# Kernel tuning notes

Hardware: AMD Instinct MI355X
Metric: run time of the kernel (lower is better)

Reference implementation:

```python
import jax, jax.numpy as jnp
import numpy as np

B, L, D, H = 2, 2048, 2048, 16
HD = D // H          # head_dim = 128
LAT = HD // 4        # latent_dim = 32


def setup_inputs() -> dict:
    key = jax.random.key(0)
    ks = jax.random.split(key, 16)
    def w(k, shape, fan_in):
        return jax.random.normal(k, shape, jnp.float32) / np.float32(np.sqrt(fan_in))
    x = jax.random.normal(ks[0], (B, L, D), jnp.float32)
    # RoPE frequencies, stored as (cos, sin) pairs: [L, HD//2, 2]
    inv_freq = 1.0 / (10000.0 ** (np.arange(0, HD, 2, dtype=np.float32) / HD))
    ang = np.outer(np.arange(L, dtype=np.float32), inv_freq)
    freqs_cis = jnp.stack([jnp.asarray(np.cos(ang)), jnp.asarray(np.sin(ang))], axis=-1)
    return dict(
        x=x, freqs_cis=freqs_cis,
        Wq=w(ks[1], (D, D), D), bq=jnp.zeros((D,), jnp.float32),
        Wk=w(ks[2], (D, D), D), bk=jnp.zeros((D,), jnp.float32),
        Wv=w(ks[3], (D, D), D), bv=jnp.zeros((D,), jnp.float32),
        Wqc=w(ks[4], (LAT, HD), HD), bqc=jnp.zeros((LAT,), jnp.float32),
        Wkc=w(ks[5], (LAT, HD), HD), bkc=jnp.zeros((LAT,), jnp.float32),
        Wvc=w(ks[6], (LAT, HD), HD), bvc=jnp.zeros((LAT,), jnp.float32),
        Wd=w(ks[7], (HD, LAT), LAT), bd=jnp.zeros((HD,), jnp.float32),
        Wo=w(ks[8], (D, D), D), bo=jnp.zeros((D,), jnp.float32),
    )


def _rope(t, freqs_cis):
    # t: [B,H,L,HD]; freqs_cis: [L, HD//2, 2] (cos, sin)
    tp = t.reshape(t.shape[:-1] + (HD // 2, 2))
    a, b = tp[..., 0], tp[..., 1]
    cr = freqs_cis[:, :, 0]  # [L, HD//2]
    ci = freqs_cis[:, :, 1]
    ra = a * cr - b * ci
    rb = a * ci + b * cr
    return jnp.stack([ra, rb], axis=-1).reshape(t.shape)


def reference(x, freqs_cis, Wq, bq, Wk, bk, Wv, bv, Wqc, bqc, Wkc, bkc, Wvc, bvc, Wd, bd, Wo, bo):
    Bx, Lx, Dx = x.shape
    # QKV projections -> [B,H,L,HD]
    def proj(W, bias):
        return (x @ W.T + bias).reshape(Bx, Lx, H, HD).transpose(0, 2, 1, 3)
    q = proj(Wq, bq)
    k = proj(Wk, bk)
    v = proj(Wv, bv)
    q = _rope(q, freqs_cis)
    k = _rope(k, freqs_cis)
    # per-head compression to latent dim: [B,H,L,LAT]
    qc = q @ Wqc.T + bqc
    kc = k @ Wkc.T + bkc
    vc = v @ Wvc.T + bvc
    scores = jnp.einsum('bhie,bhje->bhij', qc, kc) / np.float32(np.sqrt(LAT))
    mask = jnp.triu(jnp.ones((Lx, Lx), bool), 1)  # future positions
    scores = jnp.where(mask, jnp.float32(-jnp.inf), scores)
    probs = jax.nn.softmax(scores, axis=-1)
    attn = jnp.einsum('bhij,bhje->bhie', probs, vc)  # [B,H,L,LAT]
    attn = attn @ Wd.T + bd                          # decompress -> [B,H,L,HD]
    attn = attn.transpose(0, 2, 1, 3).reshape(Bx, Lx, Dx)
    return attn @ Wo.T + bo
```

## Files before the change

### kernel.cpp

```cpp
#include <hip/hip_runtime.h>

typedef __attribute__((ext_vector_type(8))) __bf16 bf16x8;
typedef __attribute__((ext_vector_type(4))) __bf16 bf16x4;
typedef __attribute__((ext_vector_type(4))) float f32x4;
typedef __attribute__((ext_vector_type(16))) float f32x16;

#define LL 2048
#define DD 2048
#define HH 16
#define HDIM 128

__global__ __launch_bounds__(256)
void cvt_all(const float* __restrict__ x, const float* __restrict__ Wq,
             const float* __restrict__ Wk, const float* __restrict__ Wqc,
             const float* __restrict__ Wkc,
             __bf16* __restrict__ xb, __bf16* __restrict__ Wqb, __bf16* __restrict__ Wkb,
             __bf16* __restrict__ Wqcb, __bf16* __restrict__ Wkcb)
{
    size_t i = (size_t)blockIdx.x * 256 + threadIdx.x;
    const float* s; __bf16* d; size_t off;
    if (i < 2097152)      { s = x;   d = xb;   off = i; }
    else if (i < 3145728) { s = Wq;  d = Wqb;  off = i - 2097152; }
    else if (i < 4194304) { s = Wk;  d = Wkb;  off = i - 3145728; }
    else if (i < 4195328) { s = Wqc; d = Wqcb; off = i - 4194304; }
    else                  { s = Wkc; d = Wkcb; off = i - 4195328; }
    float4 v = *(const float4*)(s + off * 4);
    bf16x4 o = { (__bf16)v.x, (__bf16)v.y, (__bf16)v.z, (__bf16)v.w };
    *(bf16x4*)(d + off * 4) = o;
}

__global__ __launch_bounds__(256)
void build_wv_eff(const float* __restrict__ Wv, const float* __restrict__ Wvc,
                  const float* __restrict__ bv, const float* __restrict__ bvc,
                  __bf16* __restrict__ Wveff, float* __restrict__ bveff)
{
    __shared__ float WvcT[128][32];
    const int h = blockIdx.x, dc = blockIdx.y, tid = threadIdx.x;
    for (int i = tid; i < 4096; i += 256) WvcT[i & 127][i >> 7] = Wvc[i];
    __syncthreads();
    const int d  = dc * 64 + (tid & 63);
    const int o0 = (tid >> 6) * 8;
    float acc[8] = {};
    for (int j = 0; j < 128; ++j) {
        const float w = Wv[(size_t)(h * 128 + j) * 2048 + d];
        #pragma unroll
        for (int o = 0; o < 8; ++o) acc[o] += WvcT[j][o0 + o] * w;
    }
    #pragma unroll
    for (int o = 0; o < 8; ++o)
        Wveff[(size_t)(h * 32 + o0 + o) * 2048 + d] = (__bf16)acc[o];
    if (dc == 0 && tid < 32) {
        float s = bvc[tid];
        for (int j = 0; j < 128; ++j) s += WvcT[j][tid] * bv[h * 128 + j];
        bveff[h * 32 + tid] = s;
    }
}

__global__ __launch_bounds__(256)
void build_wo_eff(const float* __restrict__ Wo, const float* __restrict__ Wd,
                  __bf16* __restrict__ Woeff)
{
    __shared__ float WdL[128][32];
    const int dc = blockIdx.x, h = blockIdx.y, tid = threadIdx.x;
    for (int i = tid; i < 4096; i += 256) WdL[i >> 5][i & 31] = Wd[i];
    __syncthreads();
    const int dout = dc * 64 + (tid & 63);
    const int o0   = (tid >> 6) * 8;
    float acc[8] = {};
    const float* wrow = Wo + (size_t)dout * 2048 + h * 128;
    for (int u = 0; u < 128; ++u) {
        const float w = wrow[u];
        #pragma unroll
        for (int o = 0; o < 8; ++o) acc[o] += WdL[u][o0 + o] * w;
    }
    #pragma unroll
    for (int o = 0; o < 8; ++o)
        Woeff[(size_t)dout * 512 + h * 32 + o0 + o] = (__bf16)acc[o];
}

__global__ __launch_bounds__(256)
void build_bo_eff(const float* __restrict__ Wo, const float* __restrict__ bd,
                  const float* __restrict__ bo, float* __restrict__ boeff)
{
    __shared__ float bdL[128];
    const int tid = threadIdx.x;
    if (tid < 128) bdL[tid] = bd[tid];
    __syncthreads();
    const int d  = blockIdx.x * 32 + (tid >> 3);
    const int s0 = (tid & 7) * 64;
    float s = 0.f;
    const float* wrow = Wo + (size_t)d * 2048 + s0 * 4;
    for (int c4 = 0; c4 < 64; ++c4) {
        float4 wv = *(const float4*)(wrow + c4 * 4);
        const int cb = ((s0 + c4) * 4) & 127;
        s += wv.x * bdL[cb] + wv.y * bdL[cb + 1] + wv.z * bdL[cb + 2] + wv.w * bdL[cb + 3];
    }
    #pragma unroll
    for (int off = 4; off; off >>= 1) s += __shfl_down(s, off, 8);
    if ((tid & 7) == 0) boeff[d] = bo[d] + s;
}

typedef unsigned int u32;
typedef const __attribute__((address_space(1))) u32* gp_t;
typedef __attribute__((address_space(3))) u32* lp_t;
__device__ __forceinline__ void gload16(const __bf16* g, __bf16* l)
{
    __builtin_amdgcn_global_load_lds((gp_t)(const void*)g, (lp_t)(void*)l, 16, 0, 0);
}

#define MF16(a, b, c) __builtin_amdgcn_mfma_f32_16x16x32_bf16(a, b, c, 0, 0, 0)

__global__ __launch_bounds__(256, 3)
void gemm_qkv(const __bf16* __restrict__ A,
              const __bf16* __restrict__ Wq, const __bf16* __restrict__ Wk,
              const __bf16* __restrict__ Wveff,
              const float* __restrict__ bq, const float* __restrict__ bk,
              const float* __restrict__ bveff,
              __bf16* __restrict__ qb, __bf16* __restrict__ kb, __bf16* __restrict__ vt)
{
    __shared__ __bf16 lds[3][2][4096];

    const int bid = blockIdx.x;
    const int xcd = bid & 7;
    const int j   = bid >> 3;
    const int bx  = j >> 2;
    const int byl = j & 3;
    const int by  = xcd * 4 + byl;
    const int m0  = by * 128;
    const int which = (bx >= 32) ? 2 : (bx >> 4);
    const int n0  = (which == 2) ? (bx - 32) * 128 : (bx & 15) * 128;
    const __bf16* W = which == 0 ? Wq : which == 1 ? Wk : Wveff;

    const int tid  = threadIdx.x;
    const int wid  = tid >> 6;
    const int lane = tid & 63;
    const int wr   = wid >> 1;
    const int wc   = wid & 1;
    const int l15  = lane & 15;
    const int l4   = lane >> 4;
    const int swz  = (l4 ^ (l15 & 3)) * 8;

    const int srl  = lane >> 2;
    const int scol = ((lane & 3) ^ (srl & 3)) * 8;
    const __bf16* gA0 = A + (size_t)(m0 + wid * 32 + srl) * 2048 + scol;
    const __bf16* gB0 = W + (size_t)(n0 + wid * 32 + srl) * 2048 + scol;

    #define STAGE(bb, kk)                                                \
    {   __bf16* dA = &lds[bb][0][wid * 1024];                            \
        __bf16* dB = &lds[bb][1][wid * 1024];                            \
        gload16(gA0 + (kk), dA);                                         \
        gload16(gA0 + (size_t)16 * 2048 + (kk), dA + 512);               \
        gload16(gB0 + (kk), dB);                                         \
        gload16(gB0 + (size_t)16 * 2048 + (kk), dB + 512);               \
    }
    #define RD_A(bb, mf) (*(const bf16x8*)&lds[bb][0][(wr * 64 + (mf) * 16 + l15) * 32 + swz])
    #define RD_B(bb, nf) (*(const bf16x8*)&lds[bb][1][(wc * 64 + (nf) * 16 + l15) * 32 + swz])

    f32x4 acc[4][4] = {};

    STAGE(0, 0) STAGE(1, 32)
    asm volatile("s_waitcnt vmcnt(4)" ::: "memory");
    __builtin_amdgcn_s_barrier();

    #define TB(RB, SB, VM, DOST, kk)                                          \
    {                                                                         \
        bf16x8 fa[4], fb[4];                                                  \
        fa[0] = RD_A(RB, 0); fa[1] = RD_A(RB, 1);                             \
        fa[2] = RD_A(RB, 2); fa[3] = RD_A(RB, 3);                             \
        fb[0] = RD_B(RB, 0); fb[1] = RD_B(RB, 1);                             \
        fb[2] = RD_B(RB, 2); fb[3] = RD_B(RB, 3);                             \
        if (DOST) STAGE(SB, kk)                                               \
        asm volatile("s_waitcnt lgkmcnt(0)" ::: "memory");                    \
        __builtin_amdgcn_sched_barrier(0);                                    \
        __builtin_amdgcn_s_setprio(1);                                        \
        _Pragma("unroll")                                                     \
        for (int mf = 0; mf < 4; ++mf)                                        \
            _Pragma("unroll")                                                 \
            for (int nf = 0; nf < 4; ++nf)                                    \
                acc[mf][nf] = MF16(fa[mf], fb[nf], acc[mf][nf]);              \
        __builtin_amdgcn_s_setprio(0);                                        \
        asm volatile("s_waitcnt vmcnt(" VM ")" ::: "memory");                 \
        __builtin_amdgcn_s_barrier();                                         \
    }

    for (int tt = 0; tt < 60; tt += 3) {
        const int kk = (tt + 2) * 32;
        TB(0, 2, "4", true, kk)
        TB(1, 0, "4", true, kk + 32)
        TB(2, 1, "4", true, kk + 64)
    }
    TB(0, 2, "4", true, 62 * 32)
    TB(1, 0, "4", true, 63 * 32)
    TB(2, 0, "0", false, 0)
    TB(0, 0, "0", false, 0)
    #undef TB
    #undef STAGE
    #undef RD_A
    #undef RD_B

    if (which < 2) {
        __bf16* C = which ? kb : qb;
        const float* bb = which ? bk : bq;
        #pragma unroll
        for (int nf = 0; nf < 4; ++nf) {
            const int col = n0 + wc * 64 + nf * 16 + l15;
            const float bv = bb[col];
            #pragma unroll
            for (int mf = 0; mf < 4; ++mf) {
                const int row0 = m0 + wr * 64 + mf * 16 + l4 * 4;
                #pragma unroll
                for (int rr = 0; rr < 4; ++rr)
                    C[(size_t)(row0 + rr) * 2048 + col] = (__bf16)(acc[mf][nf][rr] + bv);
            }
        }
    } else {
        #pragma unroll
        for (int nf = 0; nf < 4; ++nf) {
            const int ncol = n0 + wc * 64 + nf * 16 + l15;
            const float bv = bveff[ncol];
            const int hh = ncol >> 5, oo = ncol & 31;
            #pragma unroll
            for (int mf = 0; mf < 4; ++mf) {
                const int row0 = m0 + wr * 64 + mf * 16 + l4 * 4;
                const int b = row0 >> 11, l0 = row0 & 2047;
                bf16x4 pk = { (__bf16)(acc[mf][nf][0] + bv), (__bf16)(acc[mf][nf][1] + bv),
                              (__bf16)(acc[mf][nf][2] + bv), (__bf16)(acc[mf][nf][3] + bv) };
                *(bf16x4*)(vt + ((size_t)((b * 16 + hh) * 32 + oo)) * 2048 + l0) = pk;
            }
        }
    }
}

__global__ __launch_bounds__(256)
void gemm_ao(const __bf16* __restrict__ ao, const __bf16* __restrict__ Woeff,
             const float* __restrict__ boeff, float* __restrict__ out)
{
    __shared__ __bf16 As[128][64];
    __shared__ __bf16 Bs[128][64];
    const int bid = blockIdx.x;
    const int x   = bid & 7;
    const int jj  = bid >> 3;
    const int bx  = x * 2 + (jj & 1);
    const int by  = jj >> 1;
    const int m0  = by * 128;
    const int n0  = bx * 128;

    const int tid  = threadIdx.x;
    const int wave = tid >> 6;
    const int lane = tid & 63;
    const int wr   = (wave >> 1) * 64;
    const int wc   = (wave & 1) * 64;
    const int lr   = lane & 15;
    const int lk   = (lane >> 4) * 8;
    const int srow = wave * 32 + (lane >> 3);
    const int scol = (lane & 7) * 8;

    f32x4 acc[4][4] = {};
    __bf16* lA = &As[wave * 32][0];
    __bf16* lB = &Bs[wave * 32][0];
    const __bf16* Ww = Woeff + (size_t)(n0 + srow) * 512 + scol;

    for (int k0 = 0; k0 < 512; k0 += 64) {
        const int kk = k0 + scol;
        const int hblk = kk >> 5, oo = kk & 31;
        #pragma unroll
        for (int j = 0; j < 4; ++j) {
            const int r = m0 + srow + j * 8;
            const int b = r >> 11, l = r & 2047;
            gload16(ao + ((size_t)((b << 4) + hblk) * 2048 + l) * 32 + oo, lA + j * 512);
            gload16(Ww + (size_t)(j * 8) * 512 + k0, lB + j * 512);
        }
        __syncthreads();
        #pragma unroll
        for (int ks = 0; ks < 2; ++ks) {
            bf16x8 af[4], bfr[4];
            #pragma unroll
            for (int m = 0; m < 4; ++m)
                af[m] = *(const bf16x8*)(&As[wr + m * 16 + lr][ks * 32 + lk]);
            #pragma unroll
            for (int n = 0; n < 4; ++n)
                bfr[n] = *(const bf16x8*)(&Bs[wc + n * 16 + lr][ks * 32 + lk]);
            #pragma unroll
            for (int m = 0; m < 4; ++m)
                #pragma unroll
                for (int n = 0; n < 4; ++n)
                    acc[m][n] = MF16(af[m], bfr[n], acc[m][n]);
        }
        __syncthreads();
    }

    const int orow = (lane >> 4) * 4;
    #pragma unroll
    for (int n = 0; n < 4; ++n) {
        const int col = n0 + wc + n * 16 + lr;
        const float bv = boeff[col];
        #pragma unroll
        for (int m = 0; m < 4; ++m) {
            #pragma unroll
            for (int r = 0; r < 4; ++r) {
                const int row = m0 + wr + m * 16 + orow + r;
                out[(size_t)row * 2048 + col] = acc[m][n][r] + bv;
            }
        }
    }
}

__global__ __launch_bounds__(256)
void latproj_mfma(const __bf16* __restrict__ qb, const __bf16* __restrict__ kb,
                  const __bf16* __restrict__ Wqcb, const __bf16* __restrict__ Wkcb,
                  const float* __restrict__ bq, const float* __restrict__ bk,
                  const float* __restrict__ fc,
                  __bf16* __restrict__ qc, __bf16* __restrict__ kc)
{
    const int which = blockIdx.y;
    const __bf16* in = which == 0 ? qb : kb;
    const __bf16* Wb = which == 0 ? Wqcb : Wkcb;
    const float*  bs = which == 0 ? bq : bk;

    const int wave = threadIdx.x >> 6;
    const int lane = threadIdx.x & 63;
    const int o    = lane & 31;
    const int hi   = lane >> 5;
    const int g0   = (blockIdx.x * 4 + wave) * 32;

    bf16x8 wf[8];
    #pragma unroll
    for (int ks = 0; ks < 8; ++ks)
        wf[ks] = *(const bf16x8*)(Wb + o * 128 + ks * 16 + hi * 8);

    const int g = g0 + o;
    const int b = g >> 15, h = (g >> 11) & 15, l = g & (LL - 1);
    const __bf16* arow = in + ((size_t)(b * LL + l)) * DD + h * HDIM;
    const float* fcr = fc + (size_t)l * 128;

    f32x16 C = {};
    #pragma unroll
    for (int ks = 0; ks < 8; ++ks) {
        bf16x8 af = *(const bf16x8*)(arow + ks * 16 + hi * 8);
        const float4 cA = *(const float4*)(fcr + (ks * 8 + hi * 4) * 2);
        const float4 cB = *(const float4*)(fcr + (ks * 8 + hi * 4) * 2 + 4);
        float a, bb_;
        a = (float)af[0]; bb_ = (float)af[1];
        af[0] = (__bf16)(a * cA.x - bb_ * cA.y); af[1] = (__bf16)(a * cA.y + bb_ * cA.x);
        a = (float)af[2]; bb_ = (float)af[3];
        af[2] = (__bf16)(a * cA.z - bb_ * cA.w); af[3] = (__bf16)(a * cA.w + bb_ * cA.z);
        a = (float)af[4]; bb_ = (float)af[5];
        af[4] = (__bf16)(a * cB.x - bb_ * cB.y); af[5] = (__bf16)(a * cB.y + bb_ * cB.x);
        a = (float)af[6]; bb_ = (float)af[7];
        af[6] = (__bf16)(a * cB.z - bb_ * cB.w); af[7] = (__bf16)(a * cB.w + bb_ * cB.z);
        C = __builtin_amdgcn_mfma_f32_32x32x16_bf16(af, wf[ks], C, 0, 0, 0);
    }

    const float bias = bs[o];
    const float QSCALE = 0.17677669529663689f * 1.44269504088896340f;
    __bf16* outp = (which == 0 ? qc : kc);
    #pragma unroll
    for (int r = 0; r < 16; ++r) {
        const int ro = (r & 3) + 8 * (r >> 2) + 4 * hi;
        float v = C[r] + bias;
        if (which == 0) v *= QSCALE;
        outp[(size_t)(g0 + ro) * 32 + o] = (__bf16)v;
    }
}

__device__ __forceinline__ unsigned pkbf2(float a, float b)
{
    union { __bf16 h[2]; unsigned u; } x;
    x.h[0] = (__bf16)a; x.h[1] = (__bf16)b;
    return x.u;
}

#if __has_builtin(__builtin_amdgcn_permlane32_swap)
typedef unsigned int uint2v __attribute__((ext_vector_type(2)));
__device__ __forceinline__ void plswap(unsigned a, unsigned b, unsigned& w_lo, unsigned& w_hi, int)
{
    uint2v r = __builtin_amdgcn_permlane32_swap(a, b, false, false);
    w_lo = r[0]; w_hi = r[1];
}
#else
__device__ __forceinline__ void plswap(unsigned a, unsigned b, unsigned& w_lo, unsigned& w_hi, int hi)
{
    unsigned ax = (unsigned)__shfl_xor((int)a, 32);
    unsigned bx = (unsigned)__shfl_xor((int)b, 32);
    w_lo = hi ? bx : a;
    w_hi = hi ? b  : ax;
}
#endif

__global__ __launch_bounds__(64)
void attn_part(const __bf16* __restrict__ qc, const __bf16* __restrict__ kc,
               const __bf16* __restrict__ vt,
               float* __restrict__ pm, float* __restrict__ pl, float* __restrict__ po)
{
    const int id  = blockIdx.x;
    const int bhl = id & 7;
    const int c   = id >> 3;
    const int bhh = c / 160;
    const int lin = c - bhh * 160;
    int s, ci;
    if (lin < 16)      { s = lin; ci = 0; }
    else if (lin < 48) { int q = lin - 16; s = 16 + (q >> 1); ci = q & 1; }
    else if (lin < 96) { int q = lin - 48; int d = q / 3; s = 32 + d; ci = q - d * 3; }
    else               { int q = lin - 96; s = 48 + (q >> 2); ci = q & 3; }
    const int bh = bhh * 8 + bhl;

    const int lane = threadIdx.x;
    const int qcol = lane & 31;
    const int hi   = lane >> 5;

    const __bf16* qbase = qc + ((size_t)bh * LL + (size_t)s * 32) * 32;
    const __bf16* kbase = kc + (size_t)bh * LL * 32;
    const __bf16* vbase = vt + (size_t)bh * 32 * LL;

    const bf16x8 qf0 = *(const bf16x8*)(qbase + qcol * 32 + hi * 8);
    const bf16x8 qf1 = *(const bf16x8*)(qbase + qcol * 32 + 16 + hi * 8);

    float m = -1e30f, lsum = 0.f;
    f32x16 O = {};

    const int t0 = ci * 16;
    const int t1 = min(s, t0 + 15);

    const __bf16* krow = kbase + (size_t)(t0 * 32 + qcol) * 32 + hi * 8;
    const __bf16* vrow = vbase + (size_t)qcol * LL + t0 * 32 + hi * 8;
    bf16x8 kc0 = *(const bf16x8*)(krow);
    bf16x8 kc1 = *(const bf16x8*)(krow + 16);
    bf16x8 vc0 = *(const bf16x8*)(vrow);
    bf16x8 vc1 = *(const bf16x8*)(vrow + 16);

    for (int t = t0; t <= t1; ++t) {
        const int tn = (t < t1) ? t + 1 : t;
        const __bf16* krn = kbase + (size_t)(tn * 32 + qcol) * 32 + hi * 8;
        const __bf16* vrn = vbase + (size_t)qcol * LL + tn * 32 + hi * 8;
        bf16x8 kn0 = *(const bf16x8*)(krn);
        bf16x8 kn1 = *(const bf16x8*)(krn + 16);
        bf16x8 vn0 = *(const bf16x8*)(vrn);
        bf16x8 vn1 = *(const bf16x8*)(vrn + 16);

        f32x16 S = {};
        S = __builtin_amdgcn_mfma_f32_32x32x16_bf16(kc0, qf0, S, 0, 0, 0);
        S = __builtin_amdgcn_mfma_f32_32x32x16_bf16(kc1, qf1, S, 0, 0, 0);

        if (t == s) {
            #pragma unroll
            for (int r = 0; r < 16; ++r) {
                const int kl = (r & 3) + 8 * (r >> 2) + 4 * hi;
                if (kl > qcol) S[r] = -1e30f;
            }
        }
        float tm = S[0];
        #pragma unroll
        for (int r = 1; r < 16; ++r) tm = fmaxf(tm, S[r]);
        tm = fmaxf(tm, __shfl_xor(tm, 32));
        const float mn = fmaxf(m, tm);
        const float fr = exp2f(m - mn);
        m = mn;
        float p[16]; float ls = 0.f;
        #pragma unroll
        for (int r = 0; r < 16; ++r) { p[r] = exp2f(S[r] - m); ls += p[r]; }
        lsum = lsum * fr + ls;
        #pragma unroll
        for (int r = 0; r < 16; ++r) O[r] *= fr;

        unsigned w[8];
        #pragma unroll
        for (int i = 0; i < 8; ++i) w[i] = pkbf2(p[2 * i], p[2 * i + 1]);
        union PF { unsigned u[4]; bf16x8 v; } pf1, pf2;
        plswap(w[0], w[2], pf1.u[0], pf1.u[2], hi);
        plswap(w[1], w[3], pf1.u[1], pf1.u[3], hi);
        plswap(w[4], w[6], pf2.u[0], pf2.u[2], hi);
        plswap(w[5], w[7], pf2.u[1], pf2.u[3], hi);

        O = __builtin_amdgcn_mfma_f32_32x32x16_bf16(vc0, pf1.v, O, 0, 0, 0);
        O = __builtin_amdgcn_mfma_f32_32x32x16_bf16(vc1, pf2.v, O, 0, 0, 0);

        kc0 = kn0; kc1 = kn1; vc0 = vn0; vc1 = vn1;
    }

    const float L = lsum + __shfl_xor(lsum, 32);
    const size_t g = (size_t)bh * LL + (size_t)s * 32 + qcol;
    const size_t slot = g * 4 + ci;
    if (hi == 0) { pm[slot] = m; pl[slot] = L; }
    float* pp = po + slot * 32;
    #pragma unroll
    for (int g4 = 0; g4 < 4; ++g4) {
        float4 v = { O[g4 * 4 + 0], O[g4 * 4 + 1], O[g4 * 4 + 2], O[g4 * 4 + 3] };
        *(float4*)(pp + g4 * 8 + 4 * hi) = v;
    }
}

__global__ __launch_bounds__(256)
void attn_comb(const float* __restrict__ pm, const float* __restrict__ pl,
               const float* __restrict__ po, __bf16* __restrict__ ao)
{
    const int g = blockIdx.x * 256 + threadIdx.x;
    const int i = g & (LL - 1);
    const int nch = (i >> 9) + 1;
    float m = -1e30f;
    for (int c = 0; c < nch; ++c) m = fmaxf(m, pm[(size_t)g * 4 + c]);
    float L = 0.f;
    float o[32] = {};
    for (int c = 0; c < nch; ++c) {
        const float w = exp2f(pm[(size_t)g * 4 + c] - m);
        L += w * pl[(size_t)g * 4 + c];
        const float* pp = po + ((size_t)g * 4 + c) * 32;
        #pragma unroll
        for (int d4 = 0; d4 < 8; ++d4) {
            float4 v = *(const float4*)(pp + d4 * 4);
            o[d4*4+0] += w * v.x; o[d4*4+1] += w * v.y;
            o[d4*4+2] += w * v.z; o[d4*4+3] += w * v.w;
        }
    }
    const float inv = 1.f / L;
    #pragma unroll
    for (int d8 = 0; d8 < 4; ++d8) {
        bf16x8 v;
        #pragma unroll
        for (int j = 0; j < 8; ++j) v[j] = (__bf16)(o[d8 * 8 + j] * inv);
        *(bf16x8*)(ao + (size_t)g * 32 + d8 * 8) = v;
    }
}

extern "C" void kernel_launch(void* const* d_in, const int* in_sizes, int n_in,
                              void* d_out, int out_size, void* d_ws, size_t ws_size,
                              hipStream_t stream)
{
    const float* x   = (const float*)d_in[0];
    const float* fc  = (const float*)d_in[1];
    const float* Wq  = (const float*)d_in[2];
    const float* bq  = (const float*)d_in[3];
    const float* Wk  = (const float*)d_in[4];
    const float* bk  = (const float*)d_in[5];
    const float* Wv  = (const float*)d_in[6];
    const float* bv  = (const float*)d_in[7];
    const float* Wqc = (const float*)d_in[8];
    const float* bqc = (const float*)d_in[9];
    const float* Wkc = (const float*)d_in[10];
    const float* bkc = (const float*)d_in[11];
    const float* Wvc = (const float*)d_in[12];
    const float* bvc = (const float*)d_in[13];
    const float* Wd  = (const float*)d_in[14];
    const float* bd  = (const float*)d_in[15];
    const float* Wo  = (const float*)d_in[16];
    const float* bo  = (const float*)d_in[17];
    float* out = (float*)d_out;

    const size_t MB = 1048576;
    char* w = (char*)d_ws;
    __bf16* xb    = (__bf16*)(w);
    __bf16* Wqb   = (__bf16*)(w + 16 * MB);
    __bf16* Wkb   = (__bf16*)(w + 24 * MB);
    __bf16* Wveff = (__bf16*)(w + 32 * MB);
    __bf16* qb    = (__bf16*)(w + 34 * MB);
    __bf16* kb    = (__bf16*)(w + 50 * MB);
    __bf16* qcbf  = (__bf16*)(w + 66 * MB);
    __bf16* kcbf  = (__bf16*)(w + 70 * MB);
    __bf16* vtbf  = (__bf16*)(w + 74 * MB);
    __bf16* aobf  = (__bf16*)(w + 78 * MB);
    __bf16* Wqcb  = (__bf16*)(w + 82 * MB);
    __bf16* Wkcb  = (__bf16*)(w + 82 * MB + 8192);
    __bf16* Woeff = (__bf16*)(w + 83 * MB);
    float*  boeff = (float*)(w + 85 * MB);
    float*  bveff = (float*)(w + 85 * MB + 8192);

    float* po = (float*)d_ws;
    float* pm = (float*)(w + 32 * MB);
    float* pl = (float*)(w + 33 * MB);

    if (ws_size < (size_t)90 * MB) return;

    cvt_all<<<16392, 256, 0, stream>>>(x, Wq, Wk, Wqc, Wkc, xb, Wqb, Wkb, Wqcb, Wkcb);
    build_wv_eff<<<dim3(16, 32), 256, 0, stream>>>(Wv, Wvc, bv, bvc, Wveff, bveff);
    build_wo_eff<<<dim3(32, 16), 256, 0, stream>>>(Wo, Wd, Woeff);
    build_bo_eff<<<64, 256, 0, stream>>>(Wo, bd, bo, boeff);

    gemm_qkv<<<1152, 256, 0, stream>>>(xb, Wqb, Wkb, Wveff, bq, bk, bveff, qb, kb, vtbf);

    latproj_mfma<<<dim3(512, 2), 256, 0, stream>>>(qb, kb, Wqcb, Wkcb, bqc, bkc, fc,
                                                   qcbf, kcbf);

    attn_part<<<5120, 64, 0, stream>>>(qcbf, kcbf, vtbf, pm, pl, po);
    attn_comb<<<256, 256, 0, stream>>>(pm, pl, po, aobf);

    gemm_ao<<<512, 256, 0, stream>>>(aobf, Woeff, boeff, out);
}
```

Before: 237.7 us.

## Fuse RoPE and latent projection into QKV GEMM epilogue via LDS

The Q/K tiles from the QKV GEMM are staged in shared memory instead of written to global bf16 buffers. The RoPE rotation and the 128->32 latent projection then run there with MFMA, and qc/kc are written directly. This removes the separate latproj kernel and the full-size intermediate q/k writes and reads. The cost is a longer GEMM epilogue with extra LDS traffic and register pressure, which may affect occupancy.

```diff
diff --git a/kernel.cpp b/kernel.cpp
--- a/kernel.cpp
+++ b/kernel.cpp
@@ -116,7 +116,10 @@
               const __bf16* __restrict__ Wveff,
               const float* __restrict__ bq, const float* __restrict__ bk,
               const float* __restrict__ bveff,
-              __bf16* __restrict__ qb, __bf16* __restrict__ kb, __bf16* __restrict__ vt)
+              const __bf16* __restrict__ Wqcb, const __bf16* __restrict__ Wkcb,
+              const float* __restrict__ bqc, const float* __restrict__ bkc,
+              const float* __restrict__ fc,
+              __bf16* __restrict__ qc, __bf16* __restrict__ kc, __bf16* __restrict__ vt)
 {
     __shared__ __bf16 lds[3][2][4096];
 
@@ -199,19 +202,66 @@
     #undef RD_B
 
     if (which < 2) {
-        __bf16* C = which ? kb : qb;
+        __bf16* qt = &lds[0][0][0];
         const float* bb = which ? bk : bq;
         #pragma unroll
         for (int nf = 0; nf < 4; ++nf) {
-            const int col = n0 + wc * 64 + nf * 16 + l15;
-            const float bv = bb[col];
+            const int col = wc * 64 + nf * 16 + l15;
+            const float bv = bb[n0 + col];
             #pragma unroll
             for (int mf = 0; mf < 4; ++mf) {
-                const int row0 = m0 + wr * 64 + mf * 16 + l4 * 4;
+                const int row0 = wr * 64 + mf * 16 + l4 * 4;
                 #pragma unroll
                 for (int rr = 0; rr < 4; ++rr)
-                    C[(size_t)(row0 + rr) * 2048 + col] = (__bf16)(acc[mf][nf][rr] + bv);
+                    qt[(row0 + rr) * 136 + col] = (__bf16)(acc[mf][nf][rr] + bv);
             }
+        }
+        __syncthreads();
+
+        const int o   = lane & 31;
+        const int hi  = lane >> 5;
+        const int h   = bx & 15;
+        const int b   = m0 >> 11;
+        const int l0b = m0 & 2047;
+        const int lrow = wid * 32 + o;
+        const int l    = l0b + lrow;
+        const __bf16* Wb = which ? Wkcb : Wqcb;
+        const float*  bs = which ? bkc : bqc;
+        const float* fcr = fc + (size_t)l * 128;
+
+        bf16x8 wf[8];
+        #pragma unroll
+        for (int ks = 0; ks < 8; ++ks)
+            wf[ks] = *(const bf16x8*)(Wb + o * 128 + ks * 16 + hi * 8);
+
+        f32x16 C = {};
+        #pragma unroll
+        for (int ks = 0; ks < 8; ++ks) {
+            bf16x8 af = *(const bf16x8*)&qt[lrow * 136 + ks * 16 + hi * 8];
+            const float4 cA = *(const float4*)(fcr + (ks * 8 + hi * 4) * 2);
+            const float4 cB = *(const float4*)(fcr + (ks * 8 + hi * 4) * 2 + 4);
+            float a, b_;
+            a = (float)af[0]; b_ = (float)af[1];
+            af[0] = (__bf16)(a * cA.x - b_ * cA.y); af[1] = (__bf16)(a * cA.y + b_ * cA.x);
+            a = (float)af[2]; b_ = (float)af[3];
+            af[2] = (__bf16)(a * cA.z - b_ * cA.w); af[3] = (__bf16)(a * cA.w + b_ * cA.z);
+            a = (float)af[4]; b_ = (float)af[5];
+            af[4] = (__bf16)(a * cB.x - b_ * cB.y); af[5] = (__bf16)(a * cB.y + b_ * cB.x);
+            a = (float)af[6]; b_ = (float)af[7];
+            af[6] = (__bf16)(a * cB.z - b_ * cB.w); af[7] = (__bf16)(a * cB.w + b_ * cB.z);
+            C = __builtin_amdgcn_mfma_f32_32x32x16_bf16(af, wf[ks], C, 0, 0, 0);
+        }
+
+        const float bias = bs[o];
+        const float QSCALE = 0.17677669529663689f * 1.44269504088896340f;
+        __bf16* outp = which ? kc : qc;
+        const size_t g0row = (size_t)(b * 16 + h) * 2048 + l0b + wid * 32;
+        #pragma unroll
+        for (int r = 0; r < 16; ++r) {
+            const int ro = (r & 3) + 8 * (r >> 2) + 4 * hi;
+            float v = C[r] + bias;
+            if (which == 0) v *= QSCALE;
+            outp[(g0row + ro) * 32 + o] = (__bf16)v;
         }
     } else {
         #pragma unroll
@@ -302,64 +352,6 @@
                 out[(size_t)row * 2048 + col] = acc[m][n][r] + bv;
             }
         }
-    }
-}
-
-__global__ __launch_bounds__(256)
-void latproj_mfma(const __bf16* __restrict__ qb, const __bf16* __restrict__ kb,
-                  const __bf16* __restrict__ Wqcb, const __bf16* __restrict__ Wkcb,
-                  const float* __restrict__ bq, const float* __restrict__ bk,
-                  const float* __restrict__ fc,
-                  __bf16* __restrict__ qc, __bf16* __restrict__ kc)
-{
-    const int which = blockIdx.y;
-    const __bf16* in = which == 0 ? qb : kb;
-    const __bf16* Wb = which == 0 ? Wqcb : Wkcb;
-    const float*  bs = which == 0 ? bq : bk;
-
-    const int wave = threadIdx.x >> 6;
-    const int lane = threadIdx.x & 63;
-    const int o    = lane & 31;
-    const int hi   = lane >> 5;
-    const int g0   = (blockIdx.x * 4 + wave) * 32;
-
-    bf16x8 wf[8];
-    #pragma unroll
-    for (int ks = 0; ks < 8; ++ks)
-        wf[ks] = *(const bf16x8*)(Wb + o * 128 + ks * 16 + hi * 8);
-
-    const int g = g0 + o;
-    const int b = g >> 15, h = (g >> 11) & 15, l = g & (LL - 1);
-    const __bf16* arow = in + ((size_t)(b * LL + l)) * DD + h * HDIM;
-    const float* fcr = fc + (size_t)l * 128;
-
-    f32x16 C = {};
-    #pragma unroll
-    for (int ks = 0; ks < 8; ++ks) {
-        bf16x8 af = *(const bf16x8*)(arow + ks * 16 + hi * 8);
-        const float4 cA = *(const float4*)(fcr + (ks * 8 + hi * 4) * 2);
-        const float4 cB = *(const float4*)(fcr + (ks * 8 + hi * 4) * 2 + 4);
-        float a, bb_;
-        a = (float)af[0]; bb_ = (float)af[1];
-        af[0] = (__bf16)(a * cA.x - bb_ * cA.y); af[1] = (__bf16)(a * cA.y + bb_ * cA.x);
-        a = (float)af[2]; bb_ = (float)af[3];
-        af[2] = (__bf16)(a * cA.z - bb_ * cA.w); af[3] = (__bf16)(a * cA.w + bb_ * cA.z);
-        a = (float)af[4]; bb_ = (float)af[5];
-        af[4] = (__bf16)(a * cB.x - bb_ * cB.y); af[5] = (__bf16)(a * cB.y + bb_ * cB.x);
-        a = (float)af[6]; bb_ = (float)af[7];
-        af[6] = (__bf16)(a * cB.z - bb_ * cB.w); af[7] = (__bf16)(a * cB.w + bb_ * cB.z);
-        C = __builtin_amdgcn_mfma_f32_32x32x16_bf16(af, wf[ks], C, 0, 0, 0);
-    }
-
-    const float bias = bs[o];
-    const float QSCALE = 0.17677669529663689f * 1.44269504088896340f;
-    __bf16* outp = (which == 0 ? qc : kc);
-    #pragma unroll
-    for (int r = 0; r < 16; ++r) {
-        const int ro = (r & 3) + 8 * (r >> 2) + 4 * hi;
-        float v = C[r] + bias;
-        if (which == 0) v *= QSCALE;
-        outp[(size_t)(g0 + ro) * 32 + o] = (__bf16)v;
     }
 }
 
@@ -551,8 +543,6 @@
     __bf16* Wqb   = (__bf16*)(w + 16 * MB);
     __bf16* Wkb   = (__bf16*)(w + 24 * MB);
     __bf16* Wveff = (__bf16*)(w + 32 * MB);
-    __bf16* qb    = (__bf16*)(w + 34 * MB);
-    __bf16* kb    = (__bf16*)(w + 50 * MB);
     __bf16* qcbf  = (__bf16*)(w + 66 * MB);
     __bf16* kcbf  = (__bf16*)(w + 70 * MB);
     __bf16* vtbf  = (__bf16*)(w + 74 * MB);
@@ -574,10 +564,8 @@
     build_wo_eff<<<dim3(32, 16), 256, 0, stream>>>(Wo, Wd, Woeff);
     build_bo_eff<<<64, 256, 0, stream>>>(Wo, bd, bo, boeff);
 
-    gemm_qkv<<<1152, 256, 0, stream>>>(xb, Wqb, Wkb, Wveff, bq, bk, bveff, qb, kb, vtbf);
-
-    latproj_mfma<<<dim3(512, 2), 256, 0, stream>>>(qb, kb, Wqcb, Wkcb, bqc, bkc, fc,
-                                                   qcbf, kcbf);
+    gemm_qkv<<<1152, 256, 0, stream>>>(xb, Wqb, Wkb, Wveff, bq, bk, bveff,
+                                       Wqcb, Wkcb, bqc, bkc, fc, qcbf, kcbf, vtbf);
 
     attn_part<<<5120, 64, 0, stream>>>(qcbf, kcbf, vtbf, pm, pl, po);
     attn_comb<<<256, 256, 0, stream>>>(pm, pl, po, aobf);
```

Measured after the change: 225.5 us. 5.1% less time.
